# Optimization experiments

Measured on AMD Instinct MI355X. Metric: run time of the kernel, lower is better.

Reference implementation:

```python
import jax, jax.numpy as jnp
import numpy as np

NUM_HEADS = 8

def setup_inputs() -> dict:
    key = jax.random.key(0)
    ks = jax.random.split(key, 4)
    A, B, H, QD = 256, 256, 2048, 2048
    xav = (6.0 / (H + H)) ** 0.5  # xavier_uniform bound for square weights
    return {
        "q": jax.random.normal(ks[0], (A, B, H), dtype=jnp.float32),
        "k": jax.random.normal(ks[1], (B, QD), dtype=jnp.float32),
        "Wq": jax.random.uniform(ks[2], (H, H), dtype=jnp.float32, minval=-xav, maxval=xav),
        "bq": jnp.zeros((H,), dtype=jnp.float32),
        "Wk": jax.random.uniform(ks[3], (H, QD), dtype=jnp.float32, minval=-xav, maxval=xav),
        "bk": jnp.zeros((H,), dtype=jnp.float32),
    }


def reference(q, k, Wq, bq, Wk, bk):
    n = NUM_HEADS
    H = Wq.shape[0]
    c = H // n
    fact = (H / n) ** -0.5
    # Linear projections (the dominant GEMMs)
    ql = jnp.einsum('abh,oh->abo', q, Wq) + bq          # [A, B, H]
    kl = jnp.einsum('bd,od->bo', k, Wk) + bk            # [B, H]
    A, B, _ = ql.shape
    # permute(1,2,0) then reshape (scrambling reshape, faithful to torch C-order)
    qp = jnp.transpose(ql, (1, 2, 0))                   # [B, H, A]
    qh = qp.reshape(A, B, n, c)                         # [A, B, n, c]
    # k: permute(1,0) -> [H, B], unsqueeze twice -> [H, B, 1, 1], reshape
    kp = jnp.transpose(kl)[:, :, None, None]            # [H, B, 1, 1]
    kh = kp.reshape(B, n, c, 1, 1)                      # [B(q-axis), n, c, 1, 1]
    # attention map einsum; h=w=1 here
    w = jnp.einsum('bqnc,qnchw->bqnhw', qh * fact, kh)  # [A, B, n, 1, 1]
    # softmax over flattened (n*h*w) dims
    w = jax.nn.softmax(w.reshape(A, B, -1), axis=-1).reshape(w.shape)
    return w
```

## Files before the change

### kernel.cpp

```cpp
#include <hip/hip_runtime.h>
#include <stdint.h>


typedef __attribute__((ext_vector_type(8))) __bf16 bf16x8;
typedef __attribute__((ext_vector_type(4))) __bf16 bf16x4;
typedef __attribute__((ext_vector_type(4))) float f32x4;

__device__ __forceinline__ void gload_lds16(const void* g, void* l) {
  __builtin_amdgcn_global_load_lds(
      (const __attribute__((address_space(1))) uint32_t*)g,
      (__attribute__((address_space(3))) uint32_t*)l, 16, 0, 0);
}

__global__ void convert_kernel(const float* __restrict__ qin,
                               const float* __restrict__ Wq,
                               const float* __restrict__ Wk,
                               const float* __restrict__ kin,
                               void* __restrict__ q_t,
                               void* __restrict__ wq_b, void* __restrict__ wk_b,
                               void* __restrict__ k_b) {
  const int NQ0 = 33554432;
  const int NQ1 = 1048576;
  const int NQ2 = 1048576;
  const int NQ3 = 131072;
  const int TOT = NQ0 + NQ1 + NQ2 + NQ3;
  for (int i = blockIdx.x * blockDim.x + threadIdx.x; i < TOT;
       i += gridDim.x * blockDim.x) {
    if (i < NQ0) {
      float4 v = ((const float4*)qin)[i];
      const int jq = i & 511;
      const int b  = (i >> 9) & 255;
      const int c  = i >> 17;
      bf16x4 o;
      o[0] = (__bf16)v.x; o[1] = (__bf16)v.y; o[2] = (__bf16)v.z; o[3] = (__bf16)v.w;
      ((bf16x4*)q_t)[(int64_t)(((b << 8) + c) << 9) + jq] = o;
    } else {
      const float4* src; bf16x4* dst; int j;
      if (i < NQ0+NQ1)              { src = (const float4*)Wq;  dst = (bf16x4*)wq_b; j = i - NQ0; }
      else if (i < NQ0+NQ1+NQ2)     { src = (const float4*)Wk;  dst = (bf16x4*)wk_b; j = i - NQ0 - NQ1; }
      else                          { src = (const float4*)kin; dst = (bf16x4*)k_b;  j = i - NQ0 - NQ1 - NQ2; }
      float4 v = src[j];
      bf16x4 o;
      o[0] = (__bf16)v.x; o[1] = (__bf16)v.y; o[2] = (__bf16)v.z; o[3] = (__bf16)v.w;
      dst[j] = o;
    }
  }
}

__global__ __launch_bounds__(256)
void kl_kernel(const void* __restrict__ k_b, const void* __restrict__ wk_b,
               const float* __restrict__ bk, void* __restrict__ kl_t_v) {
  __shared__ char smem[32768];
  const __bf16* kb   = (const __bf16*)k_b;
  const __bf16* wkb  = (const __bf16*)wk_b;
  __bf16* kl_t = (__bf16*)kl_t_v;
  const int t = threadIdx.x, w = t >> 6, l = t & 63;
  const int ntile = blockIdx.x, mtile = blockIdx.y;
  const int wr = w >> 1, wc = w & 1;
  f32x4 acc[2][2] = {};

  auto stage = [&](int buf, int kt) {
    const int row = t >> 3;
    const int col = (((t & 7) ^ (row & 7)) << 3);
#pragma unroll
    for (int i = 0; i < 2; ++i) {
      const __bf16* ga = kb + (int64_t)(mtile*64 + i*32 + row) * 2048 + kt*64 + col;
      gload_lds16(ga, smem + buf*16384 + (i*256 + w*64)*16);
      const __bf16* gb = wkb + (int64_t)(ntile*64 + i*32 + row) * 2048 + kt*64 + col;
      gload_lds16(gb, smem + buf*16384 + 8192 + (i*256 + w*64)*16);
    }
  };

  stage(0, 0);
  __syncthreads();
  int cur = 0;
  for (int kt = 0; kt < 32; ++kt) {
    if (kt + 1 < 32) stage(cur ^ 1, kt + 1);
    const char* bA = smem + cur*16384;
    const char* bB = smem + cur*16384 + 8192;
#pragma unroll
    for (int kq = 0; kq < 2; ++kq) {
      bf16x8 a[2], b[2];
      const int g = kq*4 + (l >> 4);
#pragma unroll
      for (int mi = 0; mi < 2; ++mi) {
        const int r = wr*32 + mi*16 + (l & 15);
        a[mi] = *(const bf16x8*)(bA + r*128 + ((g ^ (r & 7)) << 4));
      }
#pragma unroll
      for (int ni = 0; ni < 2; ++ni) {
        const int r = wc*32 + ni*16 + (l & 15);
        b[ni] = *(const bf16x8*)(bB + r*128 + ((g ^ (r & 7)) << 4));
      }
#pragma unroll
      for (int mi = 0; mi < 2; ++mi)
#pragma unroll
        for (int ni = 0; ni < 2; ++ni)
          acc[mi][ni] = __builtin_amdgcn_mfma_f32_16x16x32_bf16(a[mi], b[ni], acc[mi][ni], 0, 0, 0);
    }
    __syncthreads();
    cur ^= 1;
  }

#pragma unroll
  for (int ni = 0; ni < 2; ++ni) {
    const int o = ntile*64 + wc*32 + ni*16 + (l & 15);
    const float bko = bk[o];
#pragma unroll
    for (int mi = 0; mi < 2; ++mi) {
      const int c0 = mtile*64 + wr*32 + mi*16 + (l >> 4)*4;
      bf16x4 v;
      v[0] = (__bf16)(acc[mi][ni][0] + bko);
      v[1] = (__bf16)(acc[mi][ni][1] + bko);
      v[2] = (__bf16)(acc[mi][ni][2] + bko);
      v[3] = (__bf16)(acc[mi][ni][3] + bko);
      *(bf16x4*)(kl_t + (int64_t)o*256 + c0) = v;
    }
  }
}

#define PHASE2(ABUF, BBUF, H, STAGE_STMT, VM_STMT) do {                       \
  const char* bA_ = smem + (ABUF)*32768;                                      \
  const char* bB_ = smem + 98304 + (BBUF)*32768;                              \
  bf16x8 af[8]; bf16x8 bf[4];                                                 \
  {                                                                           \
    const int g_ = (H)*4 + (l >> 4);                                          \
    _Pragma("unroll") for (int m2 = 0; m2 < 8; ++m2) {                        \
      const int r_ = wr*128 + m2*16 + (l & 15);                               \
      af[m2] = *(const bf16x8*)(bA_ + r_*128 + ((g_ ^ (r_ & 7)) << 4));       \
    }                                                                         \
    _Pragma("unroll") for (int n2 = 0; n2 < 4; ++n2) {                        \
      const int r_ = wc*64 + n2*16 + (l & 15);                                \
      bf[n2] = *(const bf16x8*)(bB_ + r_*128 + ((g_ ^ (r_ & 7)) << 4));       \
    }                                                                         \
  }                                                                           \
  STAGE_STMT;                                                                 \
  asm volatile("s_waitcnt lgkmcnt(8)" ::: "memory");                          \
  __builtin_amdgcn_s_barrier();                                               \
  asm volatile("s_waitcnt lgkmcnt(0)" ::: "memory");                          \
  __builtin_amdgcn_sched_barrier(0);                                          \
  __builtin_amdgcn_s_setprio(1);                                              \
  _Pragma("unroll") for (int m2 = 0; m2 < 8; ++m2)                            \
    _Pragma("unroll") for (int n2 = 0; n2 < 4; ++n2)                          \
      acc[m2][n2] = __builtin_amdgcn_mfma_f32_16x16x32_bf16(                  \
          af[m2], bf[n2], acc[m2][n2], 0, 0, 0);                              \
  __builtin_amdgcn_s_setprio(0);                                              \
  VM_STMT;                                                                    \
  __builtin_amdgcn_s_barrier();                                               \
} while (0)

__global__ __launch_bounds__(512, 2)
void main_kernel(const void* __restrict__ q_tv, const void* __restrict__ wq_b,
                 const float* __restrict__ bq, const void* __restrict__ kl_t_v,
                 float* __restrict__ out) {
  __shared__ char smem[163840];
  const __bf16* qt   = (const __bf16*)q_tv;
  const __bf16* wqb  = (const __bf16*)wq_b;
  const __bf16* kl_t = (const __bf16*)kl_t_v;
  const int t = threadIdx.x, w = t >> 6, l = t & 63;
  const int otile = blockIdx.x, b = blockIdx.y;
  const int wr = w >> 2, wc = w & 3;
  f32x4 acc[8][4] = {};

  auto stageA = [&](int buf, int kt, int half) {
#pragma unroll
    for (int i = 0; i < 2; ++i) {
      const int r = i*128 + half*64 + (t >> 3);
      const int sg = (t & 7) ^ (r & 7);
      const __bf16* ga = qt + (int64_t)(b*256 + r) * 2048 + kt*64 + sg*8;
      gload_lds16(ga, smem + buf*32768 + r*128 + (t & 7)*16);
    }
  };
  auto stageB = [&](int buf, int kt, int half) {
#pragma unroll
    for (int i = 0; i < 2; ++i) {
      const int row64 = t >> 3;
      const int r = i*128 + half*32 + (row64 & 31) + ((row64 >> 5) << 6);
      const int sg = (t & 7) ^ (r & 7);
      const __bf16* gb = wqb + (int64_t)(otile*256 + r) * 2048 + kt*64 + sg*8;
      gload_lds16(gb, smem + 98304 + buf*32768 + r*128 + (t & 7)*16);
    }
  };

  stageA(0, 0, 0); stageA(0, 0, 1);
  stageB(0, 0, 0); stageB(0, 0, 1);
  stageA(1, 1, 0); stageA(1, 1, 1);
  asm volatile("s_waitcnt vmcnt(4)" ::: "memory");
  __builtin_amdgcn_s_barrier();

  int ac = 0;
  for (int kt = 0; kt < 32; ++kt) {
    const int as = (ac >= 1) ? ac - 1 : ac + 2;
    const int bc = kt & 1, bs = bc ^ 1;
    const bool sA = (kt < 30), sB = (kt < 31);
    PHASE2(ac, bc, 0,
           { if (sB) { stageB(bs, kt + 1, 0); stageB(bs, kt + 1, 1); } },
           {});
    PHASE2(ac, bc, 1,
           { if (sA) { stageA(as, kt + 2, 0); stageA(as, kt + 2, 1); } },
           { if (sA)      { asm volatile("s_waitcnt vmcnt(4)" ::: "memory"); }
             else if (sB) { asm volatile("s_waitcnt vmcnt(0)" ::: "memory"); } });
    ac = (ac == 2) ? 0 : ac + 1;
  }

  float psum[4] = {0.f, 0.f, 0.f, 0.f};
#pragma unroll
  for (int ni = 0; ni < 4; ++ni) {
    const int o = otile*256 + wc*64 + ni*16 + (l & 15);
    const float bqo = bq[o];
    const __bf16* klc = kl_t + (int64_t)o * 256 + wr*128 + (l >> 4)*4;
#pragma unroll
    for (int mi = 0; mi < 8; ++mi) {
      bf16x4 kv = *(const bf16x4*)(klc + mi*16);
      psum[ni] += (acc[mi][ni][0] + bqo) * (float)kv[0]
                + (acc[mi][ni][1] + bqo) * (float)kv[1]
                + (acc[mi][ni][2] + bqo) * (float)kv[2]
                + (acc[mi][ni][3] + bqo) * (float)kv[3];
    }
  }
#pragma unroll
  for (int ni = 0; ni < 4; ++ni) {
    psum[ni] += __shfl_xor(psum[ni], 16);
    psum[ni] += __shfl_xor(psum[ni], 32);
  }
  float* red = (float*)smem;
  if (l < 16) {
#pragma unroll
    for (int ni = 0; ni < 4; ++ni)
      red[wr*256 + wc*64 + ni*16 + l] = psum[ni];
  }
  __syncthreads();
  if (t < 256) {
    const float s = 0.0625f * (red[t] + red[256 + t]);
    float m = s;
    m = fmaxf(m, __shfl_xor(m, 1));
    m = fmaxf(m, __shfl_xor(m, 2));
    m = fmaxf(m, __shfl_xor(m, 4));
    const float e = __expf(s - m);
    float sum = e;
    sum += __shfl_xor(sum, 1);
    sum += __shfl_xor(sum, 2);
    sum += __shfl_xor(sum, 4);
    out[(int64_t)b*2048 + otile*256 + t] = e / sum;
  }
}

extern "C" void kernel_launch(void* const* d_in, const int* in_sizes, int n_in,
                              void* d_out, int out_size, void* d_ws, size_t ws_size,
                              hipStream_t stream) {
  (void)in_sizes; (void)n_in; (void)out_size; (void)ws_size;
  const float* q  = (const float*)d_in[0];
  const float* k  = (const float*)d_in[1];
  const float* Wq = (const float*)d_in[2];
  const float* bq = (const float*)d_in[3];
  const float* Wk = (const float*)d_in[4];
  const float* bk = (const float*)d_in[5];
  float* out = (float*)d_out;
  char* ws = (char*)d_ws;
  void* q_t  = ws;
  void* wq_b = ws + 268435456;
  void* wk_b = ws + 268435456 + 8388608;
  void* k_b  = ws + 268435456 + 16777216;
  void* kl_t = ws + 268435456 + 17825792;

  convert_kernel<<<2048, 256, 0, stream>>>(q, Wq, Wk, k, q_t, wq_b, wk_b, k_b);
  kl_kernel<<<dim3(32, 4), 256, 0, stream>>>(k_b, wk_b, bk, kl_t);
  main_kernel<<<dim3(8, 256), 512, 0, stream>>>(q_t, wq_b, bq, kl_t, out);
}
```

Before: 673.5 us.

## Simplify main loop to one barrier per k-tile and remap blocks across XCDs

The two-phase macro with interleaved barriers, lgkmcnt waits and setprio is replaced by a single compute lambda. Both B and A stages are issued up front each iteration, and there is one vmcnt wait plus one barrier at the end. Block IDs are also remapped so the otile tiles sharing a given batch row land on the same XCD, which should improve L2 reuse of q. This removes barrier overhead, but it also drops the priority hints and the split LDS-read/MFMA overlap, so it relies on the compiler's scheduling.

```diff
diff --git a/kernel.cpp b/kernel.cpp
--- a/kernel.cpp
+++ b/kernel.cpp
@@ -119,36 +119,6 @@
   }
 }
 
-#define PHASE2(ABUF, BBUF, H, STAGE_STMT, VM_STMT) do {                       \
-  const char* bA_ = smem + (ABUF)*32768;                                      \
-  const char* bB_ = smem + 98304 + (BBUF)*32768;                              \
-  bf16x8 af[8]; bf16x8 bf[4];                                                 \
-  {                                                                           \
-    const int g_ = (H)*4 + (l >> 4);                                          \
-    _Pragma("unroll") for (int m2 = 0; m2 < 8; ++m2) {                        \
-      const int r_ = wr*128 + m2*16 + (l & 15);                               \
-      af[m2] = *(const bf16x8*)(bA_ + r_*128 + ((g_ ^ (r_ & 7)) << 4));       \
-    }                                                                         \
-    _Pragma("unroll") for (int n2 = 0; n2 < 4; ++n2) {                        \
-      const int r_ = wc*64 + n2*16 + (l & 15);                                \
-      bf[n2] = *(const bf16x8*)(bB_ + r_*128 + ((g_ ^ (r_ & 7)) << 4));       \
-    }                                                                         \
-  }                                                                           \
-  STAGE_STMT;                                                                 \
-  asm volatile("s_waitcnt lgkmcnt(8)" ::: "memory");                          \
-  __builtin_amdgcn_s_barrier();                                               \
-  asm volatile("s_waitcnt lgkmcnt(0)" ::: "memory");                          \
-  __builtin_amdgcn_sched_barrier(0);                                          \
-  __builtin_amdgcn_s_setprio(1);                                              \
-  _Pragma("unroll") for (int m2 = 0; m2 < 8; ++m2)                            \
-    _Pragma("unroll") for (int n2 = 0; n2 < 4; ++n2)                          \
-      acc[m2][n2] = __builtin_amdgcn_mfma_f32_16x16x32_bf16(                  \
-          af[m2], bf[n2], acc[m2][n2], 0, 0, 0);                              \
-  __builtin_amdgcn_s_setprio(0);                                              \
-  VM_STMT;                                                                    \
-  __builtin_amdgcn_s_barrier();                                               \
-} while (0)
-
 __global__ __launch_bounds__(512, 2)
 void main_kernel(const void* __restrict__ q_tv, const void* __restrict__ wq_b,
                  const float* __restrict__ bq, const void* __restrict__ kl_t_v,
@@ -158,7 +128,10 @@
   const __bf16* wqb  = (const __bf16*)wq_b;
   const __bf16* kl_t = (const __bf16*)kl_t_v;
   const int t = threadIdx.x, w = t >> 6, l = t & 63;
-  const int otile = blockIdx.x, b = blockIdx.y;
+  const int lid = blockIdx.x + 8 * blockIdx.y;
+  const int xcd = lid & 7, slot = lid >> 3;
+  const int otile = slot & 7;
+  const int b = ((slot >> 3) << 3) | xcd;
   const int wr = w >> 2, wc = w & 3;
   f32x4 acc[8][4] = {};
 
@@ -182,6 +155,32 @@
     }
   };
 
+  auto compute = [&](int abuf, int bbuf) {
+    const char* bA_ = smem + abuf*32768;
+    const char* bB_ = smem + 98304 + bbuf*32768;
+#pragma unroll
+    for (int h = 0; h < 2; ++h) {
+      const int g_ = h*4 + (l >> 4);
+      bf16x8 af[8], bfr[4];
+#pragma unroll
+      for (int m2 = 0; m2 < 8; ++m2) {
+        const int r_ = wr*128 + m2*16 + (l & 15);
+        af[m2] = *(const bf16x8*)(bA_ + r_*128 + ((g_ ^ (r_ & 7)) << 4));
+      }
+#pragma unroll
+      for (int n2 = 0; n2 < 4; ++n2) {
+        const int r_ = wc*64 + n2*16 + (l & 15);
+        bfr[n2] = *(const bf16x8*)(bB_ + r_*128 + ((g_ ^ (r_ & 7)) << 4));
+      }
+#pragma unroll
+      for (int m2 = 0; m2 < 8; ++m2)
+#pragma unroll
+        for (int n2 = 0; n2 < 4; ++n2)
+          acc[m2][n2] = __builtin_amdgcn_mfma_f32_16x16x32_bf16(
+              af[m2], bfr[n2], acc[m2][n2], 0, 0, 0);
+    }
+  };
+
   stageA(0, 0, 0); stageA(0, 0, 1);
   stageB(0, 0, 0); stageB(0, 0, 1);
   stageA(1, 1, 0); stageA(1, 1, 1);
@@ -190,16 +189,14 @@
 
   int ac = 0;
   for (int kt = 0; kt < 32; ++kt) {
-    const int as = (ac >= 1) ? ac - 1 : ac + 2;
+    const int as = (ac >= 1) ? ac - 1 : 2;
     const int bc = kt & 1, bs = bc ^ 1;
-    const bool sA = (kt < 30), sB = (kt < 31);
-    PHASE2(ac, bc, 0,
-           { if (sB) { stageB(bs, kt + 1, 0); stageB(bs, kt + 1, 1); } },
-           {});
-    PHASE2(ac, bc, 1,
-           { if (sA) { stageA(as, kt + 2, 0); stageA(as, kt + 2, 1); } },
-           { if (sA)      { asm volatile("s_waitcnt vmcnt(4)" ::: "memory"); }
-             else if (sB) { asm volatile("s_waitcnt vmcnt(0)" ::: "memory"); } });
+    if (kt < 31) { stageB(bs, kt + 1, 0); stageB(bs, kt + 1, 1); }
+    if (kt < 30) { stageA(as, kt + 2, 0); stageA(as, kt + 2, 1); }
+    compute(ac, bc);
+    if (kt < 30)      { asm volatile("s_waitcnt vmcnt(4)" ::: "memory"); }
+    else if (kt < 31) { asm volatile("s_waitcnt vmcnt(0)" ::: "memory"); }
+    __builtin_amdgcn_s_barrier();
     ac = (ac == 2) ? 0 : ac + 1;
   }
 
```

Result: faster. 655.7 us (-2.6%).
